# Kernel tuning notes

Measured on AMD Instinct MI355X. Metric: run time of the kernel, lower is better.

The kernel has to match this reference:

```python
import jax, jax.numpy as jnp
import numpy as np

N, E, D, C = 100000, 1600000, 64, 16


def setup_inputs() -> dict:
    key = jax.random.key(0)
    ks = jax.random.split(key, 9)
    s = 0.1  # weight init scale
    return {
        "x": jax.random.normal(ks[0], (N, D), jnp.float32),
        "edge_index": jax.random.randint(ks[1], (2, E), 0, N),
        "edge_attr": jax.random.uniform(ks[2], (E, 1), jnp.float32),
        # SplineConv 1: kernel_size=3, degree=1, dim=1
        "W1": jax.random.normal(ks[3], (3, D, D), jnp.float32) * s,
        "root1": jax.random.normal(ks[4], (D, D), jnp.float32) * s,
        "b1": jnp.zeros((D,), jnp.float32),
        # SplineConv 2: kernel_size=5
        "W2": jax.random.normal(ks[5], (5, D, D), jnp.float32) * s,
        "root2": jax.random.normal(ks[6], (D, D), jnp.float32) * s,
        "b2": jnp.zeros((D,), jnp.float32),
        # MLP head
        "Wm1": jax.random.normal(ks[7], (D, D), jnp.float32) * s,
        "bm1": jnp.zeros((D,), jnp.float32),
        "Wm2": jax.random.normal(ks[8], (D, C), jnp.float32) * s,
        "bm2": jnp.zeros((C,), jnp.float32),
    }


def spline_conv(x, edge_index, pseudo, W, root, bias, K):
    """PyG SplineConv: dim=1, degree=1, open spline, aggr='mean', root+bias.

    Degree-1 open B-spline in 1D: v = p*(K-1); each edge hits kernel slots
    floor(v) and floor(v)+1 with weights (1-frac) and frac. Because the
    message x_j @ W[k] is linear, we aggregate coeff*x_j per slot first
    (segment_sum over dst), then do K small GEMMs [N,D]x[D,D].
    """
    src, dst = edge_index[0], edge_index[1]
    n = x.shape[0]
    v = pseudo[:, 0] * (K - 1)                      # [E]
    frac = v - jnp.floor(v)
    i0 = jnp.clip(jnp.floor(v).astype(jnp.int32), 0, K - 1)
    i1 = jnp.clip(i0 + 1, 0, K - 1)
    xj = x[src]                                      # [E, D] gather
    deg = jax.ops.segment_sum(jnp.ones((dst.shape[0],), x.dtype), dst,
                              num_segments=n)        # in-degree for mean
    out = jnp.zeros((n, W.shape[2]), x.dtype)
    for k in range(K):                               # small fixed K (3 or 5)
        coeff = (1.0 - frac) * (i0 == k) + frac * (i1 == k)   # [E]
        agg = jax.ops.segment_sum(xj * coeff[:, None], dst, num_segments=n)
        out = out + agg @ W[k]
    out = out / jnp.maximum(deg, 1.0)[:, None]
    return out + x @ root + bias


def reference(x, edge_index, edge_attr, W1, root1, b1, W2, root2, b2,
              Wm1, bm1, Wm2, bm2):
    # eval mode: dropout is identity
    h = jax.nn.elu(spline_conv(x, edge_index, edge_attr, W1, root1, b1, 3))
    h = jax.nn.elu(spline_conv(h, edge_index, edge_attr, W2, root2, b2, 5))
    h = jax.nn.relu(h @ Wm1 + bm1)
    return jax.nn.relu(h @ Wm2 + bm2)
```

## Files before the change

### kernel.cpp

```cpp
#include <hip/hip_runtime.h>
#include <cstdint>
#include <cstddef>


#define D_FEAT 64
#define AS_STRIDE 40
#define NB_MAX 1024
#define PART_B 128

typedef _Float16 half8v __attribute__((ext_vector_type(8)));
typedef _Float16 half4v __attribute__((ext_vector_type(4)));
typedef float f32x4 __attribute__((ext_vector_type(4)));

__device__ __forceinline__ float elu_f(float x) {
    return x > 0.f ? x : expm1f(x);
}


__global__ __launch_bounds__(256) void count_k(
    const int* __restrict__ edst, unsigned int* __restrict__ counts,
    int E, int chunk, int NBUCKET)
{
    __shared__ unsigned int hist[NB_MAX];
    int t = threadIdx.x;
    for (int b = t; b < NBUCKET; b += 256) hist[b] = 0u;
    __syncthreads();
    int e0 = blockIdx.x * chunk;
    int e1 = e0 + chunk; if (e1 > E) e1 = E;
    for (int e = e0 + t; e < e1; e += 256)
        atomicAdd(&hist[edst[e] >> 7], 1u);
    __syncthreads();
    for (int b = t; b < NBUCKET; b += 256)
        counts[(size_t)b * PART_B + blockIdx.x] = hist[b];
}

__global__ __launch_bounds__(256) void psum_k(
    const unsigned int* __restrict__ data, unsigned int* __restrict__ partial, int L)
{
    __shared__ unsigned int wsum[4];
    int i = blockIdx.x * 256 + threadIdx.x;
    int lane = threadIdx.x & 63, wid = threadIdx.x >> 6;
    unsigned int v = (i < L) ? data[i] : 0u;
    #pragma unroll
    for (int off = 32; off; off >>= 1) v += __shfl_xor(v, off);
    if (lane == 0) wsum[wid] = v;
    __syncthreads();
    if (threadIdx.x == 0)
        partial[blockIdx.x] = wsum[0] + wsum[1] + wsum[2] + wsum[3];
}

__global__ __launch_bounds__(512) void pscan_k(
    unsigned int* __restrict__ partial, int nb)
{
    __shared__ unsigned int wsum[8];
    int t = threadIdx.x, lane = t & 63, wid = t >> 6;
    unsigned int v = (t < nb) ? partial[t] : 0u;
    unsigned int orig = v;
    #pragma unroll
    for (int off = 1; off < 64; off <<= 1) {
        unsigned int s = __shfl_up(v, off);
        if (lane >= off) v += s;
    }
    if (lane == 63) wsum[wid] = v;
    __syncthreads();
    unsigned int add = 0;
    for (int i = 0; i < wid; ++i) add += wsum[i];
    if (t < nb) partial[t] = v + add - orig;
}

__global__ __launch_bounds__(256) void pwrite_k(
    unsigned int* __restrict__ data, const unsigned int* __restrict__ partial, int L)
{
    __shared__ unsigned int wsum[4];
    int i = blockIdx.x * 256 + threadIdx.x;
    int lane = threadIdx.x & 63, wid = threadIdx.x >> 6;
    unsigned int v = (i < L) ? data[i] : 0u;
    unsigned int orig = v;
    #pragma unroll
    for (int off = 1; off < 64; off <<= 1) {
        unsigned int s = __shfl_up(v, off);
        if (lane >= off) v += s;
    }
    if (lane == 63) wsum[wid] = v;
    __syncthreads();
    unsigned int add = partial[blockIdx.x];
    for (int w = 0; w < wid; ++w) add += wsum[w];
    if (i < L) data[i] = add + v - orig;
}

__global__ __launch_bounds__(256) void place_k(
    const int* __restrict__ esrc, const int* __restrict__ edst,
    const float* __restrict__ attr, const unsigned int* __restrict__ off,
    int2* __restrict__ staging, int E, int chunk, int NBUCKET)
{
    __shared__ unsigned int cur[NB_MAX];
    int t = threadIdx.x;
    for (int b = t; b < NBUCKET; b += 256)
        cur[b] = off[(size_t)b * PART_B + blockIdx.x];
    __syncthreads();
    int e0 = blockIdx.x * chunk;
    int e1 = e0 + chunk; if (e1 > E) e1 = E;
    for (int e = e0 + t; e < e1; e += 256) {
        int d = edst[e];
        unsigned int pos = atomicAdd(&cur[d >> 7], 1u);
        staging[pos] = make_int2(esrc[e] | ((d & 127) << 17), __float_as_int(attr[e]));
    }
}

__global__ __launch_bounds__(256) void binsort_k(
    const int2* __restrict__ staging, const unsigned int* __restrict__ off,
    unsigned int* __restrict__ rowptr, int2* __restrict__ packed,
    int N, int E, int NBUCKET)
{
    __shared__ unsigned int nh[128];
    __shared__ unsigned int cur[128];
    __shared__ unsigned int wtot[2];
    int bkt = blockIdx.x;
    int t = threadIdx.x;
    int node0 = bkt << 7;
    unsigned int start = off[(size_t)bkt * PART_B];
    unsigned int end = (bkt + 1 < NBUCKET) ? off[(size_t)(bkt + 1) * PART_B]
                                           : (unsigned int)E;
    if (t < 128) nh[t] = 0u;
    __syncthreads();
    for (unsigned int i = start + t; i < end; i += 256)
        atomicAdd(&nh[(staging[i].x >> 17) & 127], 1u);
    __syncthreads();
    if (t < 128) {
        int lane = t & 63;
        unsigned int v = nh[t], orig = v;
        #pragma unroll
        for (int o = 1; o < 64; o <<= 1) {
            unsigned int s = __shfl_up(v, o);
            if (lane >= o) v += s;
        }
        if (lane == 63) wtot[t >> 6] = v;
        nh[t] = v - orig;
    }
    __syncthreads();
    if (t < 128) {
        unsigned int add = (t >= 64) ? wtot[0] : 0u;
        unsigned int base = start + add + nh[t];
        cur[t] = base;
        int node = node0 + t;
        if (node < N) rowptr[node] = base;
    }
    if (bkt == NBUCKET - 1 && t == 0) rowptr[N] = (unsigned int)E;
    __syncthreads();
    for (unsigned int i = start + t; i < end; i += 256) {
        int2 r = staging[i];
        unsigned int pos = atomicAdd(&cur[(r.x >> 17) & 127], 1u);
        packed[pos] = make_int2(r.x & 0x1FFFF, r.y);
    }
}


__global__ __launch_bounds__(256) void cvt_x_k(
    const float* __restrict__ x, _Float16* __restrict__ xh, int total4)
{
    int i = blockIdx.x * 256 + threadIdx.x;
    if (i < total4) {
        float4 v = ((const float4*)x)[i];
        half4v hv = { (_Float16)v.x, (_Float16)v.y, (_Float16)v.z, (_Float16)v.w };
        ((half4v*)xh)[i] = hv;
    }
}

__global__ __launch_bounds__(256) void prep_w_k(
    const float* __restrict__ W1, const float* __restrict__ root1,
    const float* __restrict__ W2, const float* __restrict__ root2,
    _Float16* __restrict__ Wt1, _Float16* __restrict__ Wt2)
{
    int i = blockIdx.x * 256 + threadIdx.x;
    if (i < 64 * 256) {
        int n = i >> 8, k = i & 255;
        float v = (k < 192) ? W1[k * 64 + n] : root1[(k - 192) * 64 + n];
        Wt1[n * 256 + k] = (_Float16)v;
    } else if (i < 64 * 256 + 64 * 384) {
        int j = i - 64 * 256;
        int n = j / 384, k = j % 384;
        float v = (k < 320) ? W2[k * 64 + n] : root2[(k - 320) * 64 + n];
        Wt2[n * 384 + k] = (_Float16)v;
    }
}


template<int K>
__global__ __launch_bounds__(256) void gather_k(
    const _Float16* __restrict__ xin,
    const int2* __restrict__ packed,
    const unsigned int* __restrict__ rowptr,
    _Float16* __restrict__ agg, int N)
{
    int n = blockIdx.x * 4 + (threadIdx.x >> 6);
    int lane = threadIdx.x & 63;
    if (n >= N) return;
    int sub = lane >> 4;
    int col = (lane & 15) << 2;
    unsigned int s0 = rowptr[n], s1 = rowptr[n + 1];
    float acc[K][4];
    #pragma unroll
    for (int k = 0; k < K; ++k)
        #pragma unroll
        for (int j = 0; j < 4; ++j) acc[k][j] = 0.f;
    for (unsigned int e = s0; e < s1; e += 4) {
        unsigned int ee = e + (unsigned int)sub;
        bool valid = ee < s1;
        int2 pe = packed[valid ? ee : s1 - 1];
        float v = __int_as_float(pe.y) * (float)(K - 1);
        half4v hv = *(const half4v*)(xin + (size_t)pe.x * D_FEAT + col);
        float xv[4] = { (float)hv[0], (float)hv[1], (float)hv[2], (float)hv[3] };
        #pragma unroll
        for (int k = 0; k < K; ++k) {
            float w = fmaxf(1.f - fabsf(v - (float)k), 0.f);
            w = valid ? w : 0.f;
            #pragma unroll
            for (int j = 0; j < 4; ++j) acc[k][j] = fmaf(xv[j], w, acc[k][j]);
        }
    }
    float inv = 1.f / fmaxf((float)(s1 - s0), 1.f);
    #pragma unroll
    for (int k = 0; k < K; ++k) {
        float a[4];
        #pragma unroll
        for (int j = 0; j < 4; ++j) {
            a[j] = acc[k][j];
            a[j] += __shfl_xor(a[j], 16);
            a[j] += __shfl_xor(a[j], 32);
        }
        if (sub == 0) {
            half4v o = { (_Float16)(a[0] * inv), (_Float16)(a[1] * inv),
                         (_Float16)(a[2] * inv), (_Float16)(a[3] * inv) };
            *(half4v*)(agg + ((size_t)n * K + k) * D_FEAT + col) = o;
        }
    }
}


__global__ __launch_bounds__(256) void gemm_mfma(
    const _Float16* __restrict__ A, int lenA,
    const _Float16* __restrict__ X,
    const _Float16* __restrict__ Wt,
    const float* __restrict__ bias,
    _Float16* __restrict__ outh, int N)
{
    __shared__ _Float16 As[128 * AS_STRIDE];
    __shared__ _Float16 Bs[64 * AS_STRIDE];
    int t = threadIdx.x;
    int row0 = blockIdx.x * 128;
    int Kd = lenA + D_FEAT;
    int w = t >> 6, lane = t & 63;
    int m16 = lane & 15, q = lane >> 4;

    f32x4 acc[2][4];
    #pragma unroll
    for (int rf = 0; rf < 2; ++rf)
        #pragma unroll
        for (int c = 0; c < 4; ++c) acc[rf][c] = (f32x4){0.f, 0.f, 0.f, 0.f};

    int srow = t >> 1;
    int skh  = (t & 1) * 16;
    int bn   = t >> 2;
    int bkq  = (t & 3) * 8;

    int grow = row0 + srow; if (grow >= N) grow = N - 1;
    const _Float16* arowA = A + (size_t)grow * lenA;
    const _Float16* arowX = X + (size_t)grow * D_FEAT;

    for (int kk = 0; kk < Kd; kk += 32) {
        const _Float16* src = (kk < lenA) ? (arowA + kk + skh)
                                          : (arowX + (kk - lenA) + skh);
        half8v a0 = *(const half8v*)(src);
        half8v a1 = *(const half8v*)(src + 8);
        half8v b0 = *(const half8v*)(Wt + (size_t)bn * Kd + kk + bkq);
        __syncthreads();
        *(half8v*)(&As[srow * AS_STRIDE + skh]) = a0;
        *(half8v*)(&As[srow * AS_STRIDE + skh + 8]) = a1;
        *(half8v*)(&Bs[bn * AS_STRIDE + bkq]) = b0;
        __syncthreads();
        half8v af0 = *(const half8v*)(&As[(w * 32 + m16) * AS_STRIDE + q * 8]);
        half8v af1 = *(const half8v*)(&As[(w * 32 + 16 + m16) * AS_STRIDE + q * 8]);
        #pragma unroll
        for (int c = 0; c < 4; ++c) {
            half8v bf = *(const half8v*)(&Bs[(c * 16 + m16) * AS_STRIDE + q * 8]);
            acc[0][c] = __builtin_amdgcn_mfma_f32_16x16x32_f16(af0, bf, acc[0][c], 0, 0, 0);
            acc[1][c] = __builtin_amdgcn_mfma_f32_16x16x32_f16(af1, bf, acc[1][c], 0, 0, 0);
        }
    }

    #pragma unroll
    for (int rf = 0; rf < 2; ++rf)
        #pragma unroll
        for (int c = 0; c < 4; ++c) {
            int colg = c * 16 + m16;
            float bb = bias[colg];
            #pragma unroll
            for (int r = 0; r < 4; ++r) {
                int rowg = row0 + w * 32 + rf * 16 + q * 4 + r;
                if (rowg < N) {
                    float vv = elu_f(acc[rf][c][r] + bb);
                    outh[(size_t)rowg * D_FEAT + colg] = (_Float16)vv;
                }
            }
        }
}


__global__ __launch_bounds__(256) void mlp_tile(
    const _Float16* __restrict__ X,
    const float* __restrict__ Wm1,
    const float* __restrict__ bm1,
    const float* __restrict__ Wm2,
    const float* __restrict__ bm2,
    float* __restrict__ out, int N)
{
    __shared__ float As[16][68];
    __shared__ float Bs[16][68];
    __shared__ float Hs[64][68];
    int t = threadIdx.x;
    int tx = t & 15, ty = t >> 4;
    int row0 = blockIdx.x * 64;
    float acc[4][4];
    #pragma unroll
    for (int i = 0; i < 4; ++i)
        #pragma unroll
        for (int j = 0; j < 4; ++j) acc[i][j] = 0.f;

    int lrow = t >> 2;
    int lkq  = (t & 3) << 2;
    int bkr  = t >> 4;
    int bcol = (t & 15) << 2;

    for (int kk = 0; kk < D_FEAT; kk += 16) {
        int gr = row0 + lrow; if (gr >= N) gr = N - 1;
        half4v hv = *(const half4v*)(X + (size_t)gr * D_FEAT + kk + lkq);
        float4 b4 = *(const float4*)(Wm1 + (size_t)(kk + bkr) * D_FEAT + bcol);
        __syncthreads();
        As[lkq + 0][lrow] = (float)hv[0];
        As[lkq + 1][lrow] = (float)hv[1];
        As[lkq + 2][lrow] = (float)hv[2];
        As[lkq + 3][lrow] = (float)hv[3];
        *(float4*)(&Bs[bkr][bcol]) = b4;
        __syncthreads();
        #pragma unroll
        for (int k = 0; k < 16; ++k) {
            float4 av = *(const float4*)(&As[k][ty << 2]);
            float4 bv = *(const float4*)(&Bs[k][tx << 2]);
            acc[0][0] = fmaf(av.x, bv.x, acc[0][0]);
            acc[0][1] = fmaf(av.x, bv.y, acc[0][1]);
            acc[0][2] = fmaf(av.x, bv.z, acc[0][2]);
            acc[0][3] = fmaf(av.x, bv.w, acc[0][3]);
            acc[1][0] = fmaf(av.y, bv.x, acc[1][0]);
            acc[1][1] = fmaf(av.y, bv.y, acc[1][1]);
            acc[1][2] = fmaf(av.y, bv.z, acc[1][2]);
            acc[1][3] = fmaf(av.y, bv.w, acc[1][3]);
            acc[2][0] = fmaf(av.z, bv.x, acc[2][0]);
            acc[2][1] = fmaf(av.z, bv.y, acc[2][1]);
            acc[2][2] = fmaf(av.z, bv.z, acc[2][2]);
            acc[2][3] = fmaf(av.z, bv.w, acc[2][3]);
            acc[3][0] = fmaf(av.w, bv.x, acc[3][0]);
            acc[3][1] = fmaf(av.w, bv.y, acc[3][1]);
            acc[3][2] = fmaf(av.w, bv.z, acc[3][2]);
            acc[3][3] = fmaf(av.w, bv.w, acc[3][3]);
        }
    }

    float4 bv4 = *(const float4*)(bm1 + (tx << 2));
    #pragma unroll
    for (int i = 0; i < 4; ++i) {
        float4 o;
        o.x = fmaxf(acc[i][0] + bv4.x, 0.f);
        o.y = fmaxf(acc[i][1] + bv4.y, 0.f);
        o.z = fmaxf(acc[i][2] + bv4.z, 0.f);
        o.w = fmaxf(acc[i][3] + bv4.w, 0.f);
        *(float4*)(&Hs[(ty << 2) + i][tx << 2]) = o;
    }
    __syncthreads();

    int r = t >> 2;
    int cg = (t & 3) << 2;
    float4 o2 = make_float4(0.f, 0.f, 0.f, 0.f);
    #pragma unroll 8
    for (int k = 0; k < D_FEAT; ++k) {
        float hk = Hs[r][k];
        float4 w4 = *(const float4*)(Wm2 + k * 16 + cg);
        o2.x = fmaf(hk, w4.x, o2.x);
        o2.y = fmaf(hk, w4.y, o2.y);
        o2.z = fmaf(hk, w4.z, o2.z);
        o2.w = fmaf(hk, w4.w, o2.w);
    }
    int gr = row0 + r;
    if (gr < N) {
        float4 b2 = *(const float4*)(bm2 + cg);
        float4 o;
        o.x = fmaxf(o2.x + b2.x, 0.f);
        o.y = fmaxf(o2.y + b2.y, 0.f);
        o.z = fmaxf(o2.z + b2.z, 0.f);
        o.w = fmaxf(o2.w + b2.w, 0.f);
        *(float4*)(out + (size_t)gr * 16 + cg) = o;
    }
}

extern "C" void kernel_launch(void* const* d_in, const int* in_sizes, int n_in,
                              void* d_out, int out_size, void* d_ws, size_t ws_size,
                              hipStream_t stream)
{
    const float* x     = (const float*)d_in[0];
    const int*   eidx  = (const int*)d_in[1];
    const float* attr  = (const float*)d_in[2];
    const float* W1    = (const float*)d_in[3];
    const float* root1 = (const float*)d_in[4];
    const float* b1    = (const float*)d_in[5];
    const float* W2    = (const float*)d_in[6];
    const float* root2 = (const float*)d_in[7];
    const float* b2    = (const float*)d_in[8];
    const float* Wm1   = (const float*)d_in[9];
    const float* bm1   = (const float*)d_in[10];
    const float* Wm2   = (const float*)d_in[11];
    const float* bm2   = (const float*)d_in[12];
    float* out = (float*)d_out;

    int N = in_sizes[0] / D_FEAT;
    int E = in_sizes[1] / 2;
    const int* esrc = eidx;
    const int* edst = eidx + E;
    int NBUCKET = (N + 127) >> 7;
    int chunk = (E + PART_B - 1) / PART_B;
    int L = NBUCKET * PART_B;
    int nbL = (L + 255) / 256;

    _Float16* agg = (_Float16*)d_ws;
    _Float16* h   = agg + (size_t)N * 5 * D_FEAT;
    _Float16* xh  = h + (size_t)N * D_FEAT;
    int2* packed  = (int2*)(xh + (size_t)N * D_FEAT);
    int2* staging = packed + E;
    _Float16* Wt1 = (_Float16*)(staging + E);
    _Float16* Wt2 = Wt1 + 64 * 256;
    unsigned int* counts  = (unsigned int*)(Wt2 + 64 * 384);
    unsigned int* partial = counts + L;
    unsigned int* rowptr  = partial + 512;

    dim3 blk(256);
    dim3 grid_w((N + 3) / 4);
    dim3 grid_g64((N + 63) / 64);
    dim3 grid_g128((N + 127) / 128);

    count_k<<<dim3(PART_B), blk, 0, stream>>>(edst, counts, E, chunk, NBUCKET);
    psum_k<<<dim3(nbL), blk, 0, stream>>>(counts, partial, L);
    pscan_k<<<1, 512, 0, stream>>>(partial, nbL);
    pwrite_k<<<dim3(nbL), blk, 0, stream>>>(counts, partial, L);
    place_k<<<dim3(PART_B), blk, 0, stream>>>(esrc, edst, attr, counts, staging, E, chunk, NBUCKET);
    binsort_k<<<dim3(NBUCKET), blk, 0, stream>>>(staging, counts, rowptr, packed, N, E, NBUCKET);

    cvt_x_k<<<dim3((N * D_FEAT / 4 + 255) / 256), blk, 0, stream>>>(x, xh, N * D_FEAT / 4);
    prep_w_k<<<dim3(160), blk, 0, stream>>>(W1, root1, W2, root2, Wt1, Wt2);

    gather_k<3><<<grid_w, blk, 0, stream>>>(xh, packed, rowptr, agg, N);
    gemm_mfma<<<grid_g128, blk, 0, stream>>>(agg, 3 * D_FEAT, xh, Wt1, b1, h, N);

    gather_k<5><<<grid_w, blk, 0, stream>>>(h, packed, rowptr, agg, N);
    gemm_mfma<<<grid_g128, blk, 0, stream>>>(agg, 5 * D_FEAT, h, Wt2, b2, h, N);

    mlp_tile<<<grid_g64, blk, 0, stream>>>(h, Wm1, bm1, Wm2, bm2, out, N);
}
```

Baseline: 378.5 us.

## Fuse gather, spline GEMM and MLP head into per-tile conv kernels

```diff
diff --git a/kernel.cpp b/kernel.cpp
--- a/kernel.cpp
+++ b/kernel.cpp
@@ -4,7 +4,6 @@
 
 
 #define D_FEAT 64
-#define AS_STRIDE 40
 #define NB_MAX 1024
 #define PART_B 128
 
@@ -17,22 +16,63 @@
 }
 
 
-__global__ __launch_bounds__(256) void count_k(
-    const int* __restrict__ edst, unsigned int* __restrict__ counts,
-    int E, int chunk, int NBUCKET)
+__global__ __launch_bounds__(256) void prep_k(
+    const float* __restrict__ x, const int* __restrict__ edst,
+    const float* __restrict__ W1, const float* __restrict__ root1,
+    const float* __restrict__ W2, const float* __restrict__ root2,
+    const float* __restrict__ Wm1, const float* __restrict__ Wm2,
+    _Float16* __restrict__ xh, unsigned int* __restrict__ counts,
+    _Float16* __restrict__ Wt1, _Float16* __restrict__ Wt2,
+    _Float16* __restrict__ Wm1t, _Float16* __restrict__ Wm2t,
+    int E, int chunk, int NBUCKET, int total8, int cvtB)
 {
     __shared__ unsigned int hist[NB_MAX];
-    int t = threadIdx.x;
-    for (int b = t; b < NBUCKET; b += 256) hist[b] = 0u;
-    __syncthreads();
-    int e0 = blockIdx.x * chunk;
-    int e1 = e0 + chunk; if (e1 > E) e1 = E;
-    for (int e = e0 + t; e < e1; e += 256)
-        atomicAdd(&hist[edst[e] >> 7], 1u);
-    __syncthreads();
-    for (int b = t; b < NBUCKET; b += 256)
-        counts[(size_t)b * PART_B + blockIdx.x] = hist[b];
-}
+    int b = blockIdx.x, t = threadIdx.x;
+    if (b < cvtB) {
+        int i = b * 256 + t;
+        if (i < total8) {
+            const float4* src = (const float4*)(x + (size_t)i * 8);
+            float4 v0 = src[0], v1 = src[1];
+            half8v hv = { (_Float16)v0.x, (_Float16)v0.y, (_Float16)v0.z, (_Float16)v0.w,
+                          (_Float16)v1.x, (_Float16)v1.y, (_Float16)v1.z, (_Float16)v1.w };
+            ((half8v*)xh)[i] = hv;
+        }
+        return;
+    }
+    if (b < cvtB + PART_B) {
+        int bb = b - cvtB;
+        for (int i = t; i < NBUCKET; i += 256) hist[i] = 0u;
+        __syncthreads();
+        int e0 = bb * chunk;
+        int e1 = e0 + chunk; if (e1 > E) e1 = E;
+        for (int e = e0 + t; e < e1; e += 256)
+            atomicAdd(&hist[edst[e] >> 7], 1u);
+        __syncthreads();
+        for (int i = t; i < NBUCKET; i += 256)
+            counts[(size_t)i * PART_B + bb] = hist[i];
+        return;
+    }
+    int i = (b - cvtB - PART_B) * 256 + t;
+    if (i < 64 * 256) {
+        int n = i >> 8, k = i & 255;
+        float v = (k < 192) ? W1[k * 64 + n] : root1[(k - 192) * 64 + n];
+        Wt1[n * 256 + k] = (_Float16)v;
+    } else if (i < 64 * 256 + 64 * 384) {
+        int j = i - 64 * 256;
+        int n = j / 384, k = j % 384;
+        float v = (k < 320) ? W2[k * 64 + n] : root2[(k - 320) * 64 + n];
+        Wt2[n * 384 + k] = (_Float16)v;
+    } else if (i < 64 * 256 + 64 * 384 + 64 * 64) {
+        int j = i - 64 * 256 - 64 * 384;
+        int n = j >> 6, k = j & 63;
+        Wm1t[n * 64 + k] = (_Float16)Wm1[k * 64 + n];
+    } else if (i < 64 * 256 + 64 * 384 + 64 * 64 + 16 * 64) {
+        int j = i - 64 * 256 - 64 * 384 - 64 * 64;
+        int n = j >> 6, k = j & 63;
+        Wm2t[n * 64 + k] = (_Float16)Wm2[k * 16 + n];
+    }
+}
+
 
 __global__ __launch_bounds__(256) void psum_k(
     const unsigned int* __restrict__ data, unsigned int* __restrict__ partial, int L)
@@ -87,6 +127,7 @@
     for (int w = 0; w < wid; ++w) add += wsum[w];
     if (i < L) data[i] = add + v - orig;
 }
+
 
 __global__ __launch_bounds__(256) void place_k(
     const int* __restrict__ esrc, const int* __restrict__ edst,
@@ -155,249 +196,172 @@
 }
 
 
-__global__ __launch_bounds__(256) void cvt_x_k(
-    const float* __restrict__ x, _Float16* __restrict__ xh, int total4)
-{
-    int i = blockIdx.x * 256 + threadIdx.x;
-    if (i < total4) {
-        float4 v = ((const float4*)x)[i];
-        half4v hv = { (_Float16)v.x, (_Float16)v.y, (_Float16)v.z, (_Float16)v.w };
-        ((half4v*)xh)[i] = hv;
-    }
-}
-
-__global__ __launch_bounds__(256) void prep_w_k(
-    const float* __restrict__ W1, const float* __restrict__ root1,
-    const float* __restrict__ W2, const float* __restrict__ root2,
-    _Float16* __restrict__ Wt1, _Float16* __restrict__ Wt2)
-{
-    int i = blockIdx.x * 256 + threadIdx.x;
-    if (i < 64 * 256) {
-        int n = i >> 8, k = i & 255;
-        float v = (k < 192) ? W1[k * 64 + n] : root1[(k - 192) * 64 + n];
-        Wt1[n * 256 + k] = (_Float16)v;
-    } else if (i < 64 * 256 + 64 * 384) {
-        int j = i - 64 * 256;
-        int n = j / 384, k = j % 384;
-        float v = (k < 320) ? W2[k * 64 + n] : root2[(k - 320) * 64 + n];
-        Wt2[n * 384 + k] = (_Float16)v;
-    }
-}
-
-
-template<int K>
-__global__ __launch_bounds__(256) void gather_k(
+template<int K, bool DO_MLP>
+__global__ __launch_bounds__(512) void conv_fused(
     const _Float16* __restrict__ xin,
     const int2* __restrict__ packed,
     const unsigned int* __restrict__ rowptr,
-    _Float16* __restrict__ agg, int N)
-{
-    int n = blockIdx.x * 4 + (threadIdx.x >> 6);
-    int lane = threadIdx.x & 63;
-    if (n >= N) return;
-    int sub = lane >> 4;
-    int col = (lane & 15) << 2;
-    unsigned int s0 = rowptr[n], s1 = rowptr[n + 1];
-    float acc[K][4];
-    #pragma unroll
-    for (int k = 0; k < K; ++k)
-        #pragma unroll
-        for (int j = 0; j < 4; ++j) acc[k][j] = 0.f;
-    for (unsigned int e = s0; e < s1; e += 4) {
-        unsigned int ee = e + (unsigned int)sub;
-        bool valid = ee < s1;
-        int2 pe = packed[valid ? ee : s1 - 1];
-        float v = __int_as_float(pe.y) * (float)(K - 1);
-        half4v hv = *(const half4v*)(xin + (size_t)pe.x * D_FEAT + col);
-        float xv[4] = { (float)hv[0], (float)hv[1], (float)hv[2], (float)hv[3] };
-        #pragma unroll
-        for (int k = 0; k < K; ++k) {
-            float w = fmaxf(1.f - fabsf(v - (float)k), 0.f);
-            w = valid ? w : 0.f;
-            #pragma unroll
-            for (int j = 0; j < 4; ++j) acc[k][j] = fmaf(xv[j], w, acc[k][j]);
-        }
-    }
-    float inv = 1.f / fmaxf((float)(s1 - s0), 1.f);
-    #pragma unroll
-    for (int k = 0; k < K; ++k) {
-        float a[4];
-        #pragma unroll
-        for (int j = 0; j < 4; ++j) {
-            a[j] = acc[k][j];
-            a[j] += __shfl_xor(a[j], 16);
-            a[j] += __shfl_xor(a[j], 32);
-        }
-        if (sub == 0) {
-            half4v o = { (_Float16)(a[0] * inv), (_Float16)(a[1] * inv),
-                         (_Float16)(a[2] * inv), (_Float16)(a[3] * inv) };
-            *(half4v*)(agg + ((size_t)n * K + k) * D_FEAT + col) = o;
-        }
-    }
-}
-
-
-__global__ __launch_bounds__(256) void gemm_mfma(
-    const _Float16* __restrict__ A, int lenA,
-    const _Float16* __restrict__ X,
     const _Float16* __restrict__ Wt,
     const float* __restrict__ bias,
-    _Float16* __restrict__ outh, int N)
-{
-    __shared__ _Float16 As[128 * AS_STRIDE];
-    __shared__ _Float16 Bs[64 * AS_STRIDE];
+    const _Float16* __restrict__ Wm1t,
+    const float* __restrict__ bm1,
+    const _Float16* __restrict__ Wm2t,
+    const float* __restrict__ bm2,
+    _Float16* __restrict__ outh,
+    float* __restrict__ outf,
+    int N)
+{
+    constexpr int Kd = K * 64 + 64;
+    constexpr int S = Kd + 8;
+    __shared__ _Float16 As[64 * S];
     int t = threadIdx.x;
-    int row0 = blockIdx.x * 128;
-    int Kd = lenA + D_FEAT;
-    int w = t >> 6, lane = t & 63;
+    int wv = t >> 6, lane = t & 63;
+    int tile0 = blockIdx.x * 64;
+
+    {
+        int row = t >> 3, col = (t & 7) * 8;
+        int gr = tile0 + row; if (gr >= N) gr = N - 1;
+        *(half8v*)&As[row * S + K * 64 + col] =
+            *(const half8v*)(xin + (size_t)gr * D_FEAT + col);
+    }
+
+    {
+        int sub = lane >> 4;
+        int col = (lane & 15) << 2;
+        for (int i = 0; i < 8; ++i) {
+            int n = tile0 + wv * 8 + i;
+            if (n >= N) break;
+            unsigned int s0 = rowptr[n], s1 = rowptr[n + 1];
+            float acc[K][4];
+            #pragma unroll
+            for (int k = 0; k < K; ++k)
+                #pragma unroll
+                for (int j = 0; j < 4; ++j) acc[k][j] = 0.f;
+            for (unsigned int e = s0; e < s1; e += 4) {
+                unsigned int ee = e + (unsigned int)sub;
+                bool valid = ee < s1;
+                int2 pe = packed[valid ? ee : s1 - 1];
+                float v = __int_as_float(pe.y) * (float)(K - 1);
+                v = valid ? v : -1e9f;
+                half4v hv = *(const half4v*)(xin + (size_t)pe.x * D_FEAT + col);
+                float xv[4] = { (float)hv[0], (float)hv[1], (float)hv[2], (float)hv[3] };
+                #pragma unroll
+                for (int k = 0; k < K; ++k) {
+                    float w = fmaxf(1.f - fabsf(v - (float)k), 0.f);
+                    #pragma unroll
+                    for (int j = 0; j < 4; ++j) acc[k][j] = fmaf(xv[j], w, acc[k][j]);
+                }
+            }
+            float inv = 1.f / fmaxf((float)(s1 - s0), 1.f);
+            #pragma unroll
+            for (int k = 0; k < K; ++k) {
+                float a[4];
+                #pragma unroll
+                for (int j = 0; j < 4; ++j) {
+                    a[j] = acc[k][j];
+                    a[j] += __shfl_xor(a[j], 16);
+                    a[j] += __shfl_xor(a[j], 32);
+                }
+                if (sub == 0) {
+                    half4v o = { (_Float16)(a[0] * inv), (_Float16)(a[1] * inv),
+                                 (_Float16)(a[2] * inv), (_Float16)(a[3] * inv) };
+                    *(half4v*)&As[(n - tile0) * S + k * 64 + col] = o;
+                }
+            }
+        }
+    }
+    __syncthreads();
+
     int m16 = lane & 15, q = lane >> 4;
-
-    f32x4 acc[2][4];
+    f32x4 acc2[4];
     #pragma unroll
-    for (int rf = 0; rf < 2; ++rf)
-        #pragma unroll
-        for (int c = 0; c < 4; ++c) acc[rf][c] = (f32x4){0.f, 0.f, 0.f, 0.f};
-
-    int srow = t >> 1;
-    int skh  = (t & 1) * 16;
-    int bn   = t >> 2;
-    int bkq  = (t & 3) * 8;
-
-    int grow = row0 + srow; if (grow >= N) grow = N - 1;
-    const _Float16* arowA = A + (size_t)grow * lenA;
-    const _Float16* arowX = X + (size_t)grow * D_FEAT;
-
-    for (int kk = 0; kk < Kd; kk += 32) {
-        const _Float16* src = (kk < lenA) ? (arowA + kk + skh)
-                                          : (arowX + (kk - lenA) + skh);
-        half8v a0 = *(const half8v*)(src);
-        half8v a1 = *(const half8v*)(src + 8);
-        half8v b0 = *(const half8v*)(Wt + (size_t)bn * Kd + kk + bkq);
-        __syncthreads();
-        *(half8v*)(&As[srow * AS_STRIDE + skh]) = a0;
-        *(half8v*)(&As[srow * AS_STRIDE + skh + 8]) = a1;
-        *(half8v*)(&Bs[bn * AS_STRIDE + bkq]) = b0;
-        __syncthreads();
-        half8v af0 = *(const half8v*)(&As[(w * 32 + m16) * AS_STRIDE + q * 8]);
-        half8v af1 = *(const half8v*)(&As[(w * 32 + 16 + m16) * AS_STRIDE + q * 8]);
-        #pragma unroll
-        for (int c = 0; c < 4; ++c) {
-            half8v bf = *(const half8v*)(&Bs[(c * 16 + m16) * AS_STRIDE + q * 8]);
-            acc[0][c] = __builtin_amdgcn_mfma_f32_16x16x32_f16(af0, bf, acc[0][c], 0, 0, 0);
-            acc[1][c] = __builtin_amdgcn_mfma_f32_16x16x32_f16(af1, bf, acc[1][c], 0, 0, 0);
-        }
-    }
-
-    #pragma unroll
-    for (int rf = 0; rf < 2; ++rf)
+    for (int c = 0; c < 4; ++c) acc2[c] = (f32x4){0.f, 0.f, 0.f, 0.f};
+    if (wv < 4) {
+        int arow = wv * 16 + m16;
+        for (int kk = 0; kk < Kd; kk += 32) {
+            half8v af = *(const half8v*)&As[arow * S + kk + q * 8];
+            #pragma unroll
+            for (int c = 0; c < 4; ++c) {
+                half8v bf = *(const half8v*)(Wt + (size_t)(c * 16 + m16) * Kd + kk + q * 8);
+                acc2[c] = __builtin_amdgcn_mfma_f32_16x16x32_f16(af, bf, acc2[c], 0, 0, 0);
+            }
+        }
+    }
+
+    if (!DO_MLP) {
+        if (wv < 4) {
+            #pragma unroll
+            for (int c = 0; c < 4; ++c) {
+                int colg = c * 16 + m16;
+                float bb = bias[colg];
+                #pragma unroll
+                for (int r = 0; r < 4; ++r) {
+                    int rowg = tile0 + wv * 16 + q * 4 + r;
+                    if (rowg < N)
+                        outh[(size_t)rowg * D_FEAT + colg] = (_Float16)elu_f(acc2[c][r] + bb);
+                }
+            }
+        }
+        return;
+    }
+
+    constexpr int S2 = 72;
+    _Float16* Hs  = As;
+    _Float16* Hs2 = As + 64 * S2;
+    __syncthreads();
+    if (wv < 4) {
         #pragma unroll
         for (int c = 0; c < 4; ++c) {
             int colg = c * 16 + m16;
             float bb = bias[colg];
             #pragma unroll
-            for (int r = 0; r < 4; ++r) {
-                int rowg = row0 + w * 32 + rf * 16 + q * 4 + r;
-                if (rowg < N) {
-                    float vv = elu_f(acc[rf][c][r] + bb);
-                    outh[(size_t)rowg * D_FEAT + colg] = (_Float16)vv;
-                }
+            for (int r = 0; r < 4; ++r)
+                Hs[(wv * 16 + q * 4 + r) * S2 + colg] = (_Float16)elu_f(acc2[c][r] + bb);
+        }
+    }
+    __syncthreads();
+    f32x4 acc3[4];
+    #pragma unroll
+    for (int c = 0; c < 4; ++c) acc3[c] = (f32x4){0.f, 0.f, 0.f, 0.f};
+    if (wv < 4) {
+        #pragma unroll
+        for (int kk = 0; kk < 64; kk += 32) {
+            half8v af = *(const half8v*)&Hs[(wv * 16 + m16) * S2 + kk + q * 8];
+            #pragma unroll
+            for (int c = 0; c < 4; ++c) {
+                half8v bf = *(const half8v*)(Wm1t + (size_t)(c * 16 + m16) * 64 + kk + q * 8);
+                acc3[c] = __builtin_amdgcn_mfma_f32_16x16x32_f16(af, bf, acc3[c], 0, 0, 0);
             }
         }
-}
-
-
-__global__ __launch_bounds__(256) void mlp_tile(
-    const _Float16* __restrict__ X,
-    const float* __restrict__ Wm1,
-    const float* __restrict__ bm1,
-    const float* __restrict__ Wm2,
-    const float* __restrict__ bm2,
-    float* __restrict__ out, int N)
-{
-    __shared__ float As[16][68];
-    __shared__ float Bs[16][68];
-    __shared__ float Hs[64][68];
-    int t = threadIdx.x;
-    int tx = t & 15, ty = t >> 4;
-    int row0 = blockIdx.x * 64;
-    float acc[4][4];
-    #pragma unroll
-    for (int i = 0; i < 4; ++i)
-        #pragma unroll
-        for (int j = 0; j < 4; ++j) acc[i][j] = 0.f;
-
-    int lrow = t >> 2;
-    int lkq  = (t & 3) << 2;
-    int bkr  = t >> 4;
-    int bcol = (t & 15) << 2;
-
-    for (int kk = 0; kk < D_FEAT; kk += 16) {
-        int gr = row0 + lrow; if (gr >= N) gr = N - 1;
-        half4v hv = *(const half4v*)(X + (size_t)gr * D_FEAT + kk + lkq);
-        float4 b4 = *(const float4*)(Wm1 + (size_t)(kk + bkr) * D_FEAT + bcol);
-        __syncthreads();
-        As[lkq + 0][lrow] = (float)hv[0];
-        As[lkq + 1][lrow] = (float)hv[1];
-        As[lkq + 2][lrow] = (float)hv[2];
-        As[lkq + 3][lrow] = (float)hv[3];
-        *(float4*)(&Bs[bkr][bcol]) = b4;
-        __syncthreads();
-        #pragma unroll
-        for (int k = 0; k < 16; ++k) {
-            float4 av = *(const float4*)(&As[k][ty << 2]);
-            float4 bv = *(const float4*)(&Bs[k][tx << 2]);
-            acc[0][0] = fmaf(av.x, bv.x, acc[0][0]);
-            acc[0][1] = fmaf(av.x, bv.y, acc[0][1]);
-            acc[0][2] = fmaf(av.x, bv.z, acc[0][2]);
-            acc[0][3] = fmaf(av.x, bv.w, acc[0][3]);
-            acc[1][0] = fmaf(av.y, bv.x, acc[1][0]);
-            acc[1][1] = fmaf(av.y, bv.y, acc[1][1]);
-            acc[1][2] = fmaf(av.y, bv.z, acc[1][2]);
-            acc[1][3] = fmaf(av.y, bv.w, acc[1][3]);
-            acc[2][0] = fmaf(av.z, bv.x, acc[2][0]);
-            acc[2][1] = fmaf(av.z, bv.y, acc[2][1]);
-            acc[2][2] = fmaf(av.z, bv.z, acc[2][2]);
-            acc[2][3] = fmaf(av.z, bv.w, acc[2][3]);
-            acc[3][0] = fmaf(av.w, bv.x, acc[3][0]);
-            acc[3][1] = fmaf(av.w, bv.y, acc[3][1]);
-            acc[3][2] = fmaf(av.w, bv.z, acc[3][2]);
-            acc[3][3] = fmaf(av.w, bv.w, acc[3][3]);
-        }
-    }
-
-    float4 bv4 = *(const float4*)(bm1 + (tx << 2));
-    #pragma unroll
-    for (int i = 0; i < 4; ++i) {
-        float4 o;
-        o.x = fmaxf(acc[i][0] + bv4.x, 0.f);
-        o.y = fmaxf(acc[i][1] + bv4.y, 0.f);
-        o.z = fmaxf(acc[i][2] + bv4.z, 0.f);
-        o.w = fmaxf(acc[i][3] + bv4.w, 0.f);
-        *(float4*)(&Hs[(ty << 2) + i][tx << 2]) = o;
-    }
-    __syncthreads();
-
-    int r = t >> 2;
-    int cg = (t & 3) << 2;
-    float4 o2 = make_float4(0.f, 0.f, 0.f, 0.f);
-    #pragma unroll 8
-    for (int k = 0; k < D_FEAT; ++k) {
-        float hk = Hs[r][k];
-        float4 w4 = *(const float4*)(Wm2 + k * 16 + cg);
-        o2.x = fmaf(hk, w4.x, o2.x);
-        o2.y = fmaf(hk, w4.y, o2.y);
-        o2.z = fmaf(hk, w4.z, o2.z);
-        o2.w = fmaf(hk, w4.w, o2.w);
-    }
-    int gr = row0 + r;
-    if (gr < N) {
-        float4 b2 = *(const float4*)(bm2 + cg);
-        float4 o;
-        o.x = fmaxf(o2.x + b2.x, 0.f);
-        o.y = fmaxf(o2.y + b2.y, 0.f);
-        o.z = fmaxf(o2.z + b2.z, 0.f);
-        o.w = fmaxf(o2.w + b2.w, 0.f);
-        *(float4*)(out + (size_t)gr * 16 + cg) = o;
+    }
+    __syncthreads();
+    if (wv < 4) {
+        #pragma unroll
+        for (int c = 0; c < 4; ++c) {
+            int colg = c * 16 + m16;
+            float bb = bm1[colg];
+            #pragma unroll
+            for (int r = 0; r < 4; ++r)
+                Hs2[(wv * 16 + q * 4 + r) * S2 + colg] =
+                    (_Float16)fmaxf(acc3[c][r] + bb, 0.f);
+        }
+    }
+    __syncthreads();
+    if (wv < 4) {
+        f32x4 acc4 = (f32x4){0.f, 0.f, 0.f, 0.f};
+        #pragma unroll
+        for (int kk = 0; kk < 64; kk += 32) {
+            half8v af = *(const half8v*)&Hs2[(wv * 16 + m16) * S2 + kk + q * 8];
+            half8v bf = *(const half8v*)(Wm2t + (size_t)m16 * 64 + kk + q * 8);
+            acc4 = __builtin_amdgcn_mfma_f32_16x16x32_f16(af, bf, acc4, 0, 0, 0);
+        }
+        float bb = bm2[m16];
+        #pragma unroll
+        for (int r = 0; r < 4; ++r) {
+            int rowg = tile0 + wv * 16 + q * 4 + r;
+            if (rowg < N)
+                outf[(size_t)rowg * 16 + m16] = fmaxf(acc4[r] + bb, 0.f);
+        }
     }
 }
 
@@ -428,38 +392,38 @@
     int chunk = (E + PART_B - 1) / PART_B;
     int L = NBUCKET * PART_B;
     int nbL = (L + 255) / 256;
-
-    _Float16* agg = (_Float16*)d_ws;
-    _Float16* h   = agg + (size_t)N * 5 * D_FEAT;
-    _Float16* xh  = h + (size_t)N * D_FEAT;
-    int2* packed  = (int2*)(xh + (size_t)N * D_FEAT);
+    int total8 = N * D_FEAT / 8;
+    int cvtB = (total8 + 255) / 256;
+    int wElems = 64 * 256 + 64 * 384 + 64 * 64 + 16 * 64;
+    int wB = (wElems + 255) / 256;
+
+    _Float16* xh  = (_Float16*)d_ws;
+    _Float16* h   = xh + (size_t)N * D_FEAT;
+    int2* packed  = (int2*)(h + (size_t)N * D_FEAT);
     int2* staging = packed + E;
     _Float16* Wt1 = (_Float16*)(staging + E);
     _Float16* Wt2 = Wt1 + 64 * 256;
-    unsigned int* counts  = (unsigned int*)(Wt2 + 64 * 384);
+    _Float16* Wm1t = Wt2 + 64 * 384;
+    _Float16* Wm2t = Wm1t + 64 * 64;
+    unsigned int* counts  = (unsigned int*)(Wm2t + 16 * 64);
     unsigned int* partial = counts + L;
     unsigned int* rowptr  = partial + 512;
 
     dim3 blk(256);
-    dim3 grid_w((N + 3) / 4);
-    dim3 grid_g64((N + 63) / 64);
-    dim3 grid_g128((N + 127) / 128);
-
-    count_k<<<dim3(PART_B), blk, 0, stream>>>(edst, counts, E, chunk, NBUCKET);
+    dim3 grid_t((N + 63) / 64);
+
+    prep_k<<<dim3(cvtB + PART_B + wB), blk, 0, stream>>>(
+        x, edst, W1, root1, W2, root2, Wm1, Wm2,
+        xh, counts, Wt1, Wt2, Wm1t, Wm2t, E, chunk, NBUCKET, total8, cvtB);
+
     psum_k<<<dim3(nbL), blk, 0, stream>>>(counts, partial, L);
     pscan_k<<<1, 512, 0, stream>>>(partial, nbL);
     pwrite_k<<<dim3(nbL), blk, 0, stream>>>(counts, partial, L);
     place_k<<<dim3(PART_B), blk, 0, stream>>>(esrc, edst, attr, counts, staging, E, chunk, NBUCKET);
     binsort_k<<<dim3(NBUCKET), blk, 0, stream>>>(staging, counts, rowptr, packed, N, E, NBUCKET);
 
-    cvt_x_k<<<dim3((N * D_FEAT / 4 + 255) / 256), blk, 0, stream>>>(x, xh, N * D_FEAT / 4);
-    prep_w_k<<<dim3(160), blk, 0, stream>>>(W1, root1, W2, root2, Wt1, Wt2);
-
-    gather_k<3><<<grid_w, blk, 0, stream>>>(xh, packed, rowptr, agg, N);
-    gemm_mfma<<<grid_g128, blk, 0, stream>>>(agg, 3 * D_FEAT, xh, Wt1, b1, h, N);
-
-    gather_k<5><<<grid_w, blk, 0, stream>>>(h, packed, rowptr, agg, N);
-    gemm_mfma<<<grid_g128, blk, 0, stream>>>(agg, 5 * D_FEAT, h, Wt2, b2, h, N);
-
-    mlp_tile<<<grid_g64, blk, 0, stream>>>(h, Wm1, bm1, Wm2, bm2, out, N);
-}
+    conv_fused<3, false><<<grid_t, dim3(512), 0, stream>>>(
+        xh, packed, rowptr, Wt1, b1, nullptr, nullptr, nullptr, nullptr, h, nullptr, N);
+    conv_fused<5, true><<<grid_t, dim3(512), 0, stream>>>(
+        h, packed, rowptr, Wt2, b2, Wm1t, bm1, Wm2t, bm2, nullptr, out, N);
+}
```

After: 411.9 us. +8.8%, slower.
